# Kernel optimization log

Measured on AMD Instinct MI355X. Metric: run time of the kernel, lower is better.

## Reference

```python
import jax, jax.numpy as jnp
import numpy as np

N_NODES = 50000
N_EDGES = 800000
D_IN = 128
H = 4
D_HEAD = 32
NEG_SLOPE = 0.2


def _weighted_agg(h, w, src, dst, n):
    # agg[dst] += h[src] * w  (DGL update_all with weighted_message/reduce)
    return jax.ops.segment_sum(h[src] * w[:, None], dst, num_segments=n)


def _gat_conv(h, W, al, ar, b, src, dst):
    # DGL GATConv (eval mode: dropout off), activation=None, bias=True
    n = h.shape[0]
    feat = (h @ W).reshape(n, H, D_HEAD)          # [N,H,D]
    el = jnp.sum(feat * al, axis=-1)               # [N,H]
    er = jnp.sum(feat * ar, axis=-1)               # [N,H]
    e = jax.nn.leaky_relu(el[src] + er[dst], NEG_SLOPE)  # [E,H]
    # edge softmax over incoming edges of each dst node, per head
    m = jax.ops.segment_max(e, dst, num_segments=n)      # [N,H]
    ee = jnp.exp(e - m[dst])
    s = jax.ops.segment_sum(ee, dst, num_segments=n)     # [N,H]
    alpha = ee / s[dst]                                   # [E,H]
    msg = feat[src] * alpha[:, :, None]                   # [E,H,D]
    rst = jax.ops.segment_sum(msg, dst, num_segments=n)   # [N,H,D]
    rst = rst + b.reshape(1, H, D_HEAD)
    return rst.reshape(n, H * D_HEAD)                     # flatten(1)


def setup_inputs() -> dict:
    key = jax.random.key(0)
    ks = jax.random.split(key, 12)
    inp = {
        "in_feat": jax.random.normal(ks[0], (N_NODES, D_IN), dtype=jnp.float32),
        "edge_weights": jax.random.uniform(ks[1], (N_EDGES,), dtype=jnp.float32),
        "W0": jax.random.normal(ks[2], (D_IN, H * D_HEAD), dtype=jnp.float32) * (1.0 / np.sqrt(D_IN)),
        "al0": jax.random.normal(ks[3], (H, D_HEAD), dtype=jnp.float32) * 0.1,
        "ar0": jax.random.normal(ks[4], (H, D_HEAD), dtype=jnp.float32) * 0.1,
        "b0": jnp.zeros((H * D_HEAD,), dtype=jnp.float32),
        "W1": jax.random.normal(ks[5], (H * D_HEAD, H * D_HEAD), dtype=jnp.float32) * (1.0 / np.sqrt(H * D_HEAD)),
        "al1": jax.random.normal(ks[6], (H, D_HEAD), dtype=jnp.float32) * 0.1,
        "ar1": jax.random.normal(ks[7], (H, D_HEAD), dtype=jnp.float32) * 0.1,
        "b1": jnp.zeros((H * D_HEAD,), dtype=jnp.float32),
        "src": jax.random.randint(ks[8], (N_EDGES,), 0, N_NODES, dtype=jnp.int32),
        "dst": jax.random.randint(ks[9], (N_EDGES,), 0, N_NODES, dtype=jnp.int32),
    }
    return inp


def reference(in_feat, edge_weights, W0, al0, ar0, b0, W1, al1, ar1, b1, src, dst):
    n = in_feat.shape[0]
    h = in_feat
    # hidden layer (layers[:-1]) with edge-weighted aggregation + residual + relu
    h_old = h
    h = h + _weighted_agg(h, edge_weights, src, dst, n)
    h = _gat_conv(h, W0, al0, ar0, b0, src, dst)
    h = h + h_old  # residual=True
    h = jax.nn.relu(h)
    # final layer
    h = h + _weighted_agg(h, edge_weights, src, dst, n)
    h = _gat_conv(h, W1, al1, ar1, b1, src, dst)
    return h
```

## Files before the change

### kernel.cpp

```cpp
#include <hip/hip_runtime.h>

#define NN 50000
#define NE 800000
#define D 128
#define NH 4
#define NB 391

typedef __attribute__((ext_vector_type(8))) short bf16x8;
typedef __attribute__((ext_vector_type(4))) float f32x4;

__device__ __forceinline__ float lrelu(float x){ return x > 0.f ? x : 0.2f*x; }
__device__ __forceinline__ float sel4(int h, float4 v){
  float r = v.x;
  r = (h==1)? v.y : r;
  r = (h==2)? v.z : r;
  r = (h==3)? v.w : r;
  return r;
}
__device__ __forceinline__ ushort f2bf(float f){
  union{ float f; uint i;} v; v.f=f;
  uint r = v.i + 0x7FFFu + ((v.i>>16)&1u);
  return (ushort)(r>>16);
}
__device__ __forceinline__ uint pack2bf(float x, float y){
  return (uint)f2bf(x) | ((uint)f2bf(y)<<16);
}
__device__ __forceinline__ float bflo(uint u){ return __uint_as_float(u<<16); }
__device__ __forceinline__ float bfhi(uint u){ return __uint_as_float(u & 0xffff0000u); }
__device__ __forceinline__ uint encf(float f){
  uint b = __float_as_uint(f);
  return (b & 0x80000000u) ? ~b : (b | 0x80000000u);
}
__device__ __forceinline__ float decf(uint e){
  return (e & 0x80000000u) ? __uint_as_float(e ^ 0x80000000u) : __uint_as_float(~e);
}


__global__ void k_bhist(const int* __restrict__ dst, int* __restrict__ bcnt){
  __shared__ int c[NB];
  int t = threadIdx.x;
  for (int i=t;i<NB;i+=256) c[i]=0;
  __syncthreads();
  int base = blockIdx.x*4096;
  #pragma unroll
  for (int k=0;k<16;k++){
    int i = base + k*256 + t;
    if (i<NE) atomicAdd(&c[dst[i]>>7], 1);
  }
  __syncthreads();
  for (int i=t;i<NB;i+=256){ int v=c[i]; if (v) atomicAdd(&bcnt[i], v); }
}

__global__ void k_bscan(const int* __restrict__ bcnt, int* __restrict__ boff, int* __restrict__ bcur){
  __shared__ int sd[512];
  int t = threadIdx.x;
  int own = (t<NB)? bcnt[t] : 0;
  sd[t] = own;
  __syncthreads();
  for (int off=1; off<512; off<<=1){
    int v = (t>=off)? sd[t-off] : 0;
    __syncthreads();
    sd[t] += v;
    __syncthreads();
  }
  if (t<NB){
    int excl = sd[t]-own;
    boff[t]=excl; bcur[t]=excl;
  }
  if (t==0) boff[NB]=NE;
}

__global__ void k_binscat(const int* __restrict__ src, const int* __restrict__ dst,
                          const float* __restrict__ w, int* __restrict__ bcur,
                          uint2* __restrict__ stg){
  __shared__ int cnt[NB];
  __shared__ int st[NB];
  int t = threadIdx.x;
  for (int i=t;i<NB;i+=256) cnt[i]=0;
  __syncthreads();
  int base = blockIdx.x*4096;
  #pragma unroll
  for (int k=0;k<16;k++){
    int i = base + k*256 + t;
    if (i<NE) atomicAdd(&cnt[dst[i]>>7], 1);
  }
  __syncthreads();
  for (int i=t;i<NB;i+=256){
    int c = cnt[i];
    st[i] = c ? atomicAdd(&bcur[i], c) : 0;
    cnt[i] = 0;
  }
  __syncthreads();
  #pragma unroll
  for (int k=0;k<16;k++){
    int i = base + k*256 + t;
    if (i<NE){
      int d = dst[i];
      int b = d>>7;
      int pos = st[b] + atomicAdd(&cnt[b], 1);
      stg[pos] = make_uint2((uint)src[i] | ((uint)d<<16), __float_as_uint(w[i]));
    }
  }
}

__global__ void k_bfinal(const uint2* __restrict__ stg, const int* __restrict__ boff,
                         int* __restrict__ offs, uint2* __restrict__ edge_s){
  int b = blockIdx.x, t = threadIdx.x;
  int beg = boff[b], end = boff[b+1];
  int node0 = b<<7;
  int nnode = NN - node0; if (nnode>128) nnode=128;
  __shared__ int cnt[128];
  __shared__ int cur[128];
  if (t<128) cnt[t]=0;
  __syncthreads();
  for (int j=beg+t; j<end; j+=256)
    atomicAdd(&cnt[(stg[j].x>>16)&127], 1);
  __syncthreads();
  int own = (t<128)? cnt[t] : 0;
  for (int off=1; off<128; off<<=1){
    int v = (t<128 && t>=off)? cnt[t-off] : 0;
    __syncthreads();
    if (t<128) cnt[t] += v;
    __syncthreads();
  }
  if (t<128){
    int excl = cnt[t]-own;
    cur[t] = beg + excl;
    if (t<nnode) offs[node0+t] = beg + excl;
  }
  if (b==NB-1 && t==0) offs[NN]=NE;
  __syncthreads();
  for (int j=beg+t; j<end; j+=256){
    uint2 v = stg[j];
    int pos = atomicAdd(&cur[(v.x>>16)&127], 1);
    edge_s[pos] = v;
  }
}


__global__ void k_cvt(const float* __restrict__ in, uint* __restrict__ out16, int n2){
  int i = blockIdx.x*256 + threadIdx.x;
  if (i < n2){
    float2 f = *(const float2*)&in[(size_t)i*2];
    out16[i] = pack2bf(f.x, f.y);
  }
}

__global__ void k_cvtW(const float* __restrict__ W, uint* __restrict__ Wt){
  int i = blockIdx.x*256 + threadIdx.x;
  if (i < 128*64){
    int n = i>>6, k2 = i&63;
    float a = W[(size_t)(2*k2)*128 + n];
    float b = W[(size_t)(2*k2+1)*128 + n];
    Wt[i] = pack2bf(a,b);
  }
}

__global__ void k_prep(const float* __restrict__ W0, const float* __restrict__ al0,
                       const float* __restrict__ ar0, const float* __restrict__ W1,
                       const float* __restrict__ al1, const float* __restrict__ ar1,
                       uint* __restrict__ aug0, uint* __restrict__ aug1){
  __shared__ float sv[128][4];
  int b = blockIdx.x, t = threadIdx.x;
  const float* W = (b<2)? W0 : W1;
  const float* a = (b==0)? al0 : (b==1)? ar0 : (b==2)? al1 : ar1;
  uint* o = (b<2)? aug0 : aug1;
  int rbase = (b&1)? 132 : 128;
  int d = t>>2, h = t&3;
  float s = 0.f;
  #pragma unroll
  for (int i=0;i<32;i++) s += W[d*128 + h*32 + i] * a[h*32 + i];
  sv[d][h] = s;
  __syncthreads();
  if (t<256){
    int h2 = t>>6, k2 = t&63;
    o[(rbase+h2)*64 + k2] = pack2bf(sv[2*k2][h2], sv[2*k2+1][h2]);
  }
}

__global__ void k_wagg(const float* __restrict__ hinF, const uint* __restrict__ hin16,
                       const int* __restrict__ offs, const uint2* __restrict__ edge_s,
                       uint* __restrict__ xout16){
  int node = (blockIdx.x*256 + threadIdx.x)>>6;
  int lane = threadIdx.x & 63;
  if (node>=NN) return;
  int beg=offs[node], end=offs[node+1];
  int half = lane>>5, li = lane&31;
  float a0=0.f,a1=0.f,a2=0.f,a3=0.f;
  if (half==0){
    if (hinF){
      float4 s4 = *(const float4*)&hinF[(size_t)node*D + li*4];
      a0=s4.x; a1=s4.y; a2=s4.z; a3=s4.w;
    } else {
      uint2 su = *(const uint2*)&hin16[(size_t)node*64 + li*2];
      a0=bflo(su.x); a1=bfhi(su.x); a2=bflo(su.y); a3=bfhi(su.y);
    }
  }
  for (int cb=beg; cb<end; cb+=64){
    int n = end-cb; if (n>64) n=64;
    int idx = cb + (lane<n ? lane : n-1);
    uint2 ed = edge_s[idx];
    int sp = (int)(ed.x & 0xffffu);
    float wp = __uint_as_float(ed.y);
    int iters = (n+1)>>1;
    for (int i0=0; i0<iters; i0+=8){
      uint2 u[8]; float wk[8];
      #pragma unroll
      for (int k=0;k<8;k++){
        int q = 2*(i0+k) + half;
        int sj = __shfl(sp, q & 63);
        float wq = __shfl(wp, q & 63);
        wk[k] = (q<n)? wq : 0.f;
        u[k] = *(const uint2*)&hin16[(size_t)sj*64 + li*2];
      }
      #pragma unroll
      for (int k=0;k<8;k++){
        a0 = fmaf(bflo(u[k].x), wk[k], a0);
        a1 = fmaf(bfhi(u[k].x), wk[k], a1);
        a2 = fmaf(bflo(u[k].y), wk[k], a2);
        a3 = fmaf(bfhi(u[k].y), wk[k], a3);
      }
    }
  }
  a0 += __shfl_xor(a0,32); a1 += __shfl_xor(a1,32);
  a2 += __shfl_xor(a2,32); a3 += __shfl_xor(a3,32);
  if (half==0){
    uint2 o; o.x = pack2bf(a0,a1); o.y = pack2bf(a2,a3);
    *(uint2*)&xout16[(size_t)node*64 + li*2] = o;
  }
}

__global__ __launch_bounds__(256) void k_gemm(const uint* __restrict__ X16, const uint* __restrict__ Wtaug,
    uint* __restrict__ feat16, float* __restrict__ el, float* __restrict__ er,
    uint* __restrict__ gmax_u){
  __shared__ uint sX[128*64];
  __shared__ uint sW[144*64];
  __shared__ float sgm[4][4];
  int t = threadIdx.x;
  int row0 = blockIdx.x*128;
  #pragma unroll
  for (int i=0;i<8;i++){
    int idx = t + 256*i;
    int r = idx>>4, cb = idx&15;
    int gr = row0 + r;
    uint4 v = make_uint4(0u,0u,0u,0u);
    if (gr < NN) v = *(const uint4*)&X16[(size_t)gr*64 + cb*4];
    *(uint4*)&sX[r*64 + ((cb*4) ^ ((r&7)<<2))] = v;
  }
  #pragma unroll
  for (int i=0;i<9;i++){
    int idx = t + 256*i;
    int r = idx>>4, cb = idx&15;
    uint4 v = *(const uint4*)&Wtaug[(size_t)r*64 + cb*4];
    *(uint4*)&sW[r*64 + ((cb*4) ^ ((r&7)<<2))] = v;
  }
  __syncthreads();
  int w = t>>6, l = t&63;
  int lr = l&15, lk = l>>4;
  f32x4 acc[2][8];
  f32x4 acc_e[2];
  #pragma unroll
  for (int rf=0;rf<2;rf++){
    acc_e[rf] = (f32x4){0.f,0.f,0.f,0.f};
    #pragma unroll
    for (int cf=0;cf<8;cf++) acc[rf][cf] = (f32x4){0.f,0.f,0.f,0.f};
  }
  #pragma unroll
  for (int ks=0; ks<4; ks++){
    int cb = ks*4 + lk;
    bf16x8 a[2], b[8], baug;
    #pragma unroll
    for (int rf=0;rf<2;rf++){
      int r = w*32 + rf*16 + lr;
      a[rf] = *(const bf16x8*)&sX[r*64 + ((cb*4) ^ ((r&7)<<2))];
    }
    #pragma unroll
    for (int cf=0;cf<8;cf++){
      int r = cf*16 + lr;
      b[cf] = *(const bf16x8*)&sW[r*64 + ((cb*4) ^ ((r&7)<<2))];
    }
    {
      int r = 128 + lr;
      baug = *(const bf16x8*)&sW[r*64 + ((cb*4) ^ ((r&7)<<2))];
    }
    #pragma unroll
    for (int rf=0;rf<2;rf++){
      #pragma unroll
      for (int cf=0;cf<8;cf++)
        acc[rf][cf] = __builtin_amdgcn_mfma_f32_16x16x32_bf16(a[rf], b[cf], acc[rf][cf], 0,0,0);
      acc_e[rf] = __builtin_amdgcn_mfma_f32_16x16x32_bf16(a[rf], baug, acc_e[rf], 0,0,0);
    }
  }
  ushort* f16s = (ushort*)feat16;
  float gm = -3e38f;
  #pragma unroll
  for (int rf=0;rf<2;rf++){
    #pragma unroll
    for (int reg=0;reg<4;reg++){
      int grow = row0 + w*32 + rf*16 + lk*4 + reg;
      if (grow < NN){
        #pragma unroll
        for (int cf=0;cf<8;cf++)
          f16s[(size_t)grow*128 + cf*16 + lr] = f2bf(acc[rf][cf][reg]);
        float v = acc_e[rf][reg];
        if (lr<4){ el[grow*4 + lr] = v; gm = fmaxf(gm, v); }
        else if (lr<8){ er[grow*4 + lr-4] = v; }
      }
    }
  }
  gm = fmaxf(gm, __shfl_xor(gm,16));
  gm = fmaxf(gm, __shfl_xor(gm,32));
  if (l<4) sgm[w][l] = gm;
  __syncthreads();
  if (t<4){
    float m = fmaxf(fmaxf(sgm[0][t],sgm[1][t]), fmaxf(sgm[2][t],sgm[3][t]));
    atomicMax(&gmax_u[t], encf(m));
  }
}

template<int FINAL>
__global__ void k_gat(const uint* __restrict__ feat16, const float4* __restrict__ el4,
                      const float4* __restrict__ er4, const uint* __restrict__ gmax_u,
                      const float* __restrict__ bias, const int* __restrict__ offs,
                      const uint2* __restrict__ edge_s, const float* __restrict__ resid,
                      float* __restrict__ outF, uint* __restrict__ out16){
  int node = (blockIdx.x*256 + threadIdx.x)>>6;
  int lane = threadIdx.x & 63;
  if (node>=NN) return;
  int beg=offs[node], end=offs[node+1];
  int half = lane>>5, li = lane&31;
  int hF = li>>3;
  int hp = lane & 3;
  int eidx = lane>>2;
  float4 erv = er4[node];
  uint4 g = *(const uint4*)gmax_u;
  float4 m4 = make_float4(lrelu(decf(g.x)+erv.x), lrelu(decf(g.y)+erv.y),
                          lrelu(decf(g.z)+erv.z), lrelu(decf(g.w)+erv.w));
  float mh  = sel4(hp, m4);
  float erh = sel4(hp, erv);
  float s_acc = 0.f;
  float a0=0.f,a1=0.f,a2=0.f,a3=0.f;
  for (int cb=beg; cb<end; cb+=16){
    int n = end-cb; if (n>16) n=16;
    int jj = cb + (eidx<n ? eidx : n-1);
    uint2 ed = edge_s[jj];
    int sp = (int)(ed.x & 0xffffu);
    float4 ev = el4[sp];
    float e = __expf(lrelu(sel4(hp,ev)+erh) - mh);
    e = (eidx<n) ? e : 0.f;
    s_acc += e;
    uint2 u[8]; float eh[8];
    #pragma unroll
    for (int k=0;k<8;k++){
      int bidx = (2*k + half)<<2;
      int sj = __shfl(sp, bidx);
      eh[k] = __shfl(e, bidx + hF);
      u[k] = *(const uint2*)&feat16[(size_t)sj*64 + li*2];
    }
    #pragma unroll
    for (int k=0;k<8;k++){
      a0 = fmaf(bflo(u[k].x), eh[k], a0);
      a1 = fmaf(bfhi(u[k].x), eh[k], a1);
      a2 = fmaf(bflo(u[k].y), eh[k], a2);
      a3 = fmaf(bfhi(u[k].y), eh[k], a3);
    }
  }
  s_acc += __shfl_xor(s_acc,4);
  s_acc += __shfl_xor(s_acc,8);
  s_acc += __shfl_xor(s_acc,16);
  s_acc += __shfl_xor(s_acc,32);
  float sh = __shfl(s_acc, hF);
  a0 += __shfl_xor(a0,32); a1 += __shfl_xor(a1,32);
  a2 += __shfl_xor(a2,32); a3 += __shfl_xor(a3,32);
  if (half==0){
    float inv = (end>beg)? 1.f/sh : 0.f;
    float4 bv = *(const float4*)&bias[li*4];
    float r0 = a0*inv + bv.x;
    float r1 = a1*inv + bv.y;
    float r2 = a2*inv + bv.z;
    float r3 = a3*inv + bv.w;
    if (FINAL==0){
      float4 rs = *(const float4*)&resid[(size_t)node*D + li*4];
      r0 = fmaxf(r0+rs.x, 0.f);
      r1 = fmaxf(r1+rs.y, 0.f);
      r2 = fmaxf(r2+rs.z, 0.f);
      r3 = fmaxf(r3+rs.w, 0.f);
      uint2 o16; o16.x = pack2bf(r0,r1); o16.y = pack2bf(r2,r3);
      *(uint2*)&out16[(size_t)node*64 + li*2] = o16;
    } else {
      *(float4*)&outF[(size_t)node*D + li*4] = make_float4(r0,r1,r2,r3);
    }
  }
}

extern "C" void kernel_launch(void* const* d_in, const int* in_sizes, int n_in,
                              void* d_out, int out_size, void* d_ws, size_t ws_size,
                              hipStream_t stream){
  const float* in_feat = (const float*)d_in[0];
  const float* ew  = (const float*)d_in[1];
  const float* W0  = (const float*)d_in[2];
  const float* al0 = (const float*)d_in[3];
  const float* ar0 = (const float*)d_in[4];
  const float* b0  = (const float*)d_in[5];
  const float* W1  = (const float*)d_in[6];
  const float* al1 = (const float*)d_in[7];
  const float* ar1 = (const float*)d_in[8];
  const float* b1  = (const float*)d_in[9];
  const int* src = (const int*)d_in[10];
  const int* dst = (const int*)d_in[11];
  float* out = (float*)d_out;

  char* p = (char*)d_ws;
  auto alloc = [&](size_t b)->void*{ void* r=(void*)p; p += ((b+255)&~(size_t)255); return r; };
  int*   offs   = (int*)alloc((size_t)(NN+1)*4);
  int*   bcnt   = (int*)alloc((size_t)NB*4);
  int*   boff   = (int*)alloc((size_t)(NB+1)*4);
  int*   bcur   = (int*)alloc((size_t)NB*4);
  uint2* stg    = (uint2*)alloc((size_t)NE*8);
  uint2* edge_s = (uint2*)alloc((size_t)NE*8);
  uint*  h16    = (uint*)alloc((size_t)NN*64*4);
  uint*  x16    = (uint*)alloc((size_t)NN*64*4);
  uint*  feat16 = (uint*)alloc((size_t)NN*64*4);
  uint*  Wt0    = (uint*)alloc((size_t)144*64*4);
  uint*  Wt1    = (uint*)alloc((size_t)144*64*4);
  float* el     = (float*)alloc((size_t)NN*NH*4);
  float* er     = (float*)alloc((size_t)NN*NH*4);
  uint*  gmax0  = (uint*)alloc(16);
  uint*  gmax1  = (uint*)alloc(16);

  hipMemsetAsync(bcnt, 0, (size_t)NB*4, stream);
  hipMemsetAsync(gmax0, 0, 16, stream);
  hipMemsetAsync(gmax1, 0, 16, stream);
  hipMemsetAsync(Wt0, 0, (size_t)144*64*4, stream);
  hipMemsetAsync(Wt1, 0, (size_t)144*64*4, stream);
  int nsb = (NE + 4095)/4096;
  k_bhist<<<nsb,256,0,stream>>>(dst, bcnt);
  k_bscan<<<1,512,0,stream>>>(bcnt, boff, bcur);
  k_binscat<<<nsb,256,0,stream>>>(src, dst, ew, bcur, stg);
  k_bfinal<<<NB,256,0,stream>>>(stg, boff, offs, edge_s);
  k_cvt<<<(NN*64+255)/256,256,0,stream>>>(in_feat, h16, NN*64);
  k_cvtW<<<(128*64+255)/256,256,0,stream>>>(W0, Wt0);
  k_cvtW<<<(128*64+255)/256,256,0,stream>>>(W1, Wt1);
  k_prep<<<4,512,0,stream>>>(W0, al0, ar0, W1, al1, ar1, Wt0, Wt1);

  int nwb = (NN*64 + 255)/256;
  int ngb = (NN+127)/128;

  k_wagg<<<nwb,256,0,stream>>>(in_feat, h16, offs, edge_s, x16);
  k_gemm<<<ngb,256,0,stream>>>(x16, Wt0, feat16, el, er, gmax0);
  k_gat<0><<<nwb,256,0,stream>>>(feat16, (const float4*)el, (const float4*)er, gmax0, b0,
                                 offs, edge_s, in_feat, nullptr, h16);
  k_wagg<<<nwb,256,0,stream>>>(nullptr, h16, offs, edge_s, x16);
  k_gemm<<<ngb,256,0,stream>>>(x16, Wt1, feat16, el, er, gmax1);
  k_gat<1><<<nwb,256,0,stream>>>(feat16, (const float4*)el, (const float4*)er, gmax1, b1,
                                 offs, edge_s, nullptr, out, nullptr);
}
```

Before: 234.8 us.

## Slice feature aggregation by column chunks and split GAT softmax into separate pass

Aggregation kernels are rewritten so each block handles one 16-column slice (32 bytes) of four nodes, with blockIdx ordered so consecutive blocks cover different slices. The aim is to shrink the working set of gathered rows per pass and improve L2 locality. Edges are compacted to 4-byte src|fp16-weight words. GAT softmax weights are precomputed per head into an fp16 packed array by a new k_soft kernel. This adds an extra pass and extra global traffic, and fp16 weights lose some precision.

```diff
diff --git a/kernel.cpp b/kernel.cpp
--- a/kernel.cpp
+++ b/kernel.cpp
@@ -1,4 +1,5 @@
 #include <hip/hip_runtime.h>
+#include <hip/hip_fp16.h>
 
 #define NN 50000
 #define NE 800000
@@ -34,6 +35,8 @@
 __device__ __forceinline__ float decf(uint e){
   return (e & 0x80000000u) ? __uint_as_float(e ^ 0x80000000u) : __uint_as_float(~e);
 }
+__device__ __forceinline__ uint f2h(float f){ return (uint)__half_as_ushort(__float2half(f)); }
+__device__ __forceinline__ float h2f(uint u){ return __half2float(__ushort_as_half((ushort)u)); }
 
 
 __global__ void k_bhist(const int* __restrict__ dst, int* __restrict__ bcnt){
@@ -104,7 +107,7 @@
 }
 
 __global__ void k_bfinal(const uint2* __restrict__ stg, const int* __restrict__ boff,
-                         int* __restrict__ offs, uint2* __restrict__ edge_s){
+                         int* __restrict__ offs, uint* __restrict__ wpack){
   int b = blockIdx.x, t = threadIdx.x;
   int beg = boff[b], end = boff[b+1];
   int node0 = b<<7;
@@ -133,17 +136,18 @@
   for (int j=beg+t; j<end; j+=256){
     uint2 v = stg[j];
     int pos = atomicAdd(&cur[(v.x>>16)&127], 1);
-    edge_s[pos] = v;
-  }
-}
-
-
-__global__ void k_cvt(const float* __restrict__ in, uint* __restrict__ out16, int n2){
-  int i = blockIdx.x*256 + threadIdx.x;
-  if (i < n2){
-    float2 f = *(const float2*)&in[(size_t)i*2];
-    out16[i] = pack2bf(f.x, f.y);
-  }
+    wpack[pos] = (v.x & 0xffffu) | (f2h(__uint_as_float(v.y))<<16);
+  }
+}
+
+
+__global__ void k_cvt_slice(const float* __restrict__ in, uint* __restrict__ out16){
+  int slice = blockIdx.x & 7;
+  int id = (blockIdx.x>>3)*256 + threadIdx.x;
+  if (id >= NN*8) return;
+  int v = id>>3, cp = id&7;
+  float2 f = *(const float2*)&in[(size_t)v*D + slice*16 + cp*2];
+  out16[(size_t)v*64 + slice*8 + cp] = pack2bf(f.x, f.y);
 }
 
 __global__ void k_cvtW(const float* __restrict__ W, uint* __restrict__ Wt){
@@ -178,56 +182,40 @@
   }
 }
 
-__global__ void k_wagg(const float* __restrict__ hinF, const uint* __restrict__ hin16,
-                       const int* __restrict__ offs, const uint2* __restrict__ edge_s,
-                       uint* __restrict__ xout16){
-  int node = (blockIdx.x*256 + threadIdx.x)>>6;
+__global__ void k_wagg_slice(const float* __restrict__ hinF, const uint* __restrict__ hin16,
+                             const int* __restrict__ offs, const uint* __restrict__ wpack,
+                             uint* __restrict__ x16){
+  int slice = blockIdx.x & 7;
+  int node = ((blockIdx.x>>3)<<2) + (threadIdx.x>>6);
   int lane = threadIdx.x & 63;
   if (node>=NN) return;
+  int eg = lane>>3, cp = lane&7;
   int beg=offs[node], end=offs[node+1];
-  int half = lane>>5, li = lane&31;
-  float a0=0.f,a1=0.f,a2=0.f,a3=0.f;
-  if (half==0){
+  uint co = (uint)slice*32 + cp*4;
+  const char* hb = (const char*)hin16;
+  float a0=0.f, a1=0.f;
+  if (eg==0){
     if (hinF){
-      float4 s4 = *(const float4*)&hinF[(size_t)node*D + li*4];
-      a0=s4.x; a1=s4.y; a2=s4.z; a3=s4.w;
+      float2 s2 = *(const float2*)&hinF[(size_t)node*D + slice*16 + cp*2];
+      a0=s2.x; a1=s2.y;
     } else {
-      uint2 su = *(const uint2*)&hin16[(size_t)node*64 + li*2];
-      a0=bflo(su.x); a1=bfhi(su.x); a2=bflo(su.y); a3=bfhi(su.y);
-    }
-  }
-  for (int cb=beg; cb<end; cb+=64){
-    int n = end-cb; if (n>64) n=64;
-    int idx = cb + (lane<n ? lane : n-1);
-    uint2 ed = edge_s[idx];
-    int sp = (int)(ed.x & 0xffffu);
-    float wp = __uint_as_float(ed.y);
-    int iters = (n+1)>>1;
-    for (int i0=0; i0<iters; i0+=8){
-      uint2 u[8]; float wk[8];
-      #pragma unroll
-      for (int k=0;k<8;k++){
-        int q = 2*(i0+k) + half;
-        int sj = __shfl(sp, q & 63);
-        float wq = __shfl(wp, q & 63);
-        wk[k] = (q<n)? wq : 0.f;
-        u[k] = *(const uint2*)&hin16[(size_t)sj*64 + li*2];
-      }
-      #pragma unroll
-      for (int k=0;k<8;k++){
-        a0 = fmaf(bflo(u[k].x), wk[k], a0);
-        a1 = fmaf(bfhi(u[k].x), wk[k], a1);
-        a2 = fmaf(bflo(u[k].y), wk[k], a2);
-        a3 = fmaf(bfhi(u[k].y), wk[k], a3);
-      }
-    }
-  }
+      uint su = hin16[(size_t)node*64 + slice*8 + cp];
+      a0=bflo(su); a1=bfhi(su);
+    }
+  }
+  for (int cb=beg; cb<end; cb+=8){
+    int j = cb + eg;
+    uint wp = wpack[j<end ? j : end-1];
+    float w = (j<end)? h2f(wp>>16) : 0.f;
+    uint u = *(const uint*)(hb + ((wp & 0xffffu)*256u + co));
+    a0 = fmaf(bflo(u), w, a0);
+    a1 = fmaf(bfhi(u), w, a1);
+  }
+  a0 += __shfl_xor(a0,8);  a1 += __shfl_xor(a1,8);
+  a0 += __shfl_xor(a0,16); a1 += __shfl_xor(a1,16);
   a0 += __shfl_xor(a0,32); a1 += __shfl_xor(a1,32);
-  a2 += __shfl_xor(a2,32); a3 += __shfl_xor(a3,32);
-  if (half==0){
-    uint2 o; o.x = pack2bf(a0,a1); o.y = pack2bf(a2,a3);
-    *(uint2*)&xout16[(size_t)node*64 + li*2] = o;
-  }
+  if (eg==0)
+    x16[(size_t)node*64 + slice*8 + cp] = pack2bf(a0,a1);
 }
 
 __global__ __launch_bounds__(256) void k_gemm(const uint* __restrict__ X16, const uint* __restrict__ Wtaug,
@@ -318,20 +306,15 @@
   }
 }
 
-template<int FINAL>
-__global__ void k_gat(const uint* __restrict__ feat16, const float4* __restrict__ el4,
-                      const float4* __restrict__ er4, const uint* __restrict__ gmax_u,
-                      const float* __restrict__ bias, const int* __restrict__ offs,
-                      const uint2* __restrict__ edge_s, const float* __restrict__ resid,
-                      float* __restrict__ outF, uint* __restrict__ out16){
+__global__ void k_soft(const int* __restrict__ offs, const uint* __restrict__ wpack,
+                       const float4* __restrict__ el4, const float4* __restrict__ er4,
+                       const uint* __restrict__ gmax_u,
+                       uint* __restrict__ epack, float* __restrict__ s4){
   int node = (blockIdx.x*256 + threadIdx.x)>>6;
   int lane = threadIdx.x & 63;
   if (node>=NN) return;
+  int eidx = lane>>2, hp = lane&3;
   int beg=offs[node], end=offs[node+1];
-  int half = lane>>5, li = lane&31;
-  int hF = li>>3;
-  int hp = lane & 3;
-  int eidx = lane>>2;
   float4 erv = er4[node];
   uint4 g = *(const uint4*)gmax_u;
   float4 m4 = make_float4(lrelu(decf(g.x)+erv.x), lrelu(decf(g.y)+erv.y),
@@ -339,56 +322,62 @@
   float mh  = sel4(hp, m4);
   float erh = sel4(hp, erv);
   float s_acc = 0.f;
-  float a0=0.f,a1=0.f,a2=0.f,a3=0.f;
   for (int cb=beg; cb<end; cb+=16){
     int n = end-cb; if (n>16) n=16;
-    int jj = cb + (eidx<n ? eidx : n-1);
-    uint2 ed = edge_s[jj];
-    int sp = (int)(ed.x & 0xffffu);
-    float4 ev = el4[sp];
-    float e = __expf(lrelu(sel4(hp,ev)+erh) - mh);
-    e = (eidx<n) ? e : 0.f;
-    s_acc += e;
-    uint2 u[8]; float eh[8];
-    #pragma unroll
-    for (int k=0;k<8;k++){
-      int bidx = (2*k + half)<<2;
-      int sj = __shfl(sp, bidx);
-      eh[k] = __shfl(e, bidx + hF);
-      u[k] = *(const uint2*)&feat16[(size_t)sj*64 + li*2];
-    }
-    #pragma unroll
-    for (int k=0;k<8;k++){
-      a0 = fmaf(bflo(u[k].x), eh[k], a0);
-      a1 = fmaf(bfhi(u[k].x), eh[k], a1);
-      a2 = fmaf(bflo(u[k].y), eh[k], a2);
-      a3 = fmaf(bfhi(u[k].y), eh[k], a3);
+    int j = cb + (eidx<n ? eidx : n-1);
+    uint src = wpack[j] & 0xffffu;
+    float e = __expf(lrelu(sel4(hp, el4[src])+erh) - mh);
+    if (eidx<n){
+      s_acc += e;
+      epack[hp*NE + j] = src | (f2h(e)<<16);
     }
   }
   s_acc += __shfl_xor(s_acc,4);
   s_acc += __shfl_xor(s_acc,8);
   s_acc += __shfl_xor(s_acc,16);
   s_acc += __shfl_xor(s_acc,32);
-  float sh = __shfl(s_acc, hF);
+  if (lane<4) s4[node*4 + lane] = s_acc;
+}
+
+template<int FINAL>
+__global__ void k_gat_slice(const uint* __restrict__ feat16, const uint* __restrict__ epack,
+                            const float* __restrict__ s4, const float* __restrict__ bias,
+                            const int* __restrict__ offs, const float* __restrict__ resid,
+                            float* __restrict__ outF, uint* __restrict__ out16){
+  int slice = blockIdx.x & 7;
+  int node = ((blockIdx.x>>3)<<2) + (threadIdx.x>>6);
+  int lane = threadIdx.x & 63;
+  if (node>=NN) return;
+  int eg = lane>>3, cp = lane&7;
+  int head = slice>>1;
+  const uint* ep = epack + (size_t)head*NE;
+  int beg=offs[node], end=offs[node+1];
+  uint co = (uint)slice*32 + cp*4;
+  const char* fbb = (const char*)feat16;
+  float a0=0.f, a1=0.f;
+  for (int cb=beg; cb<end; cb+=8){
+    int j = cb + eg;
+    uint pk = ep[j<end ? j : end-1];
+    float e = (j<end)? h2f(pk>>16) : 0.f;
+    uint u = *(const uint*)(fbb + ((pk & 0xffffu)*256u + co));
+    a0 = fmaf(bflo(u), e, a0);
+    a1 = fmaf(bfhi(u), e, a1);
+  }
+  a0 += __shfl_xor(a0,8);  a1 += __shfl_xor(a1,8);
+  a0 += __shfl_xor(a0,16); a1 += __shfl_xor(a1,16);
   a0 += __shfl_xor(a0,32); a1 += __shfl_xor(a1,32);
-  a2 += __shfl_xor(a2,32); a3 += __shfl_xor(a3,32);
-  if (half==0){
-    float inv = (end>beg)? 1.f/sh : 0.f;
-    float4 bv = *(const float4*)&bias[li*4];
-    float r0 = a0*inv + bv.x;
-    float r1 = a1*inv + bv.y;
-    float r2 = a2*inv + bv.z;
-    float r3 = a3*inv + bv.w;
+  if (eg==0){
+    float inv = (end>beg)? 1.f/s4[node*4 + head] : 0.f;
+    int col = slice*16 + cp*2;
+    float r0 = a0*inv + bias[col];
+    float r1 = a1*inv + bias[col+1];
     if (FINAL==0){
-      float4 rs = *(const float4*)&resid[(size_t)node*D + li*4];
+      float2 rs = *(const float2*)&resid[(size_t)node*D + col];
       r0 = fmaxf(r0+rs.x, 0.f);
       r1 = fmaxf(r1+rs.y, 0.f);
-      r2 = fmaxf(r2+rs.z, 0.f);
-      r3 = fmaxf(r3+rs.w, 0.f);
-      uint2 o16; o16.x = pack2bf(r0,r1); o16.y = pack2bf(r2,r3);
-      *(uint2*)&out16[(size_t)node*64 + li*2] = o16;
+      out16[(size_t)node*64 + slice*8 + cp] = pack2bf(r0,r1);
     } else {
-      *(float4*)&outF[(size_t)node*D + li*4] = make_float4(r0,r1,r2,r3);
+      *(float2*)&outF[(size_t)node*D + col] = make_float2(r0,r1);
     }
   }
 }
@@ -417,7 +406,9 @@
   int*   boff   = (int*)alloc((size_t)(NB+1)*4);
   int*   bcur   = (int*)alloc((size_t)NB*4);
   uint2* stg    = (uint2*)alloc((size_t)NE*8);
-  uint2* edge_s = (uint2*)alloc((size_t)NE*8);
+  uint*  wpack  = (uint*)alloc((size_t)NE*4);
+  uint*  epack  = (uint*)alloc((size_t)NE*4*NH);
+  float* s4     = (float*)alloc((size_t)NN*NH*4);
   uint*  h16    = (uint*)alloc((size_t)NN*64*4);
   uint*  x16    = (uint*)alloc((size_t)NN*64*4);
   uint*  feat16 = (uint*)alloc((size_t)NN*64*4);
@@ -437,21 +428,23 @@
   k_bhist<<<nsb,256,0,stream>>>(dst, bcnt);
   k_bscan<<<1,512,0,stream>>>(bcnt, boff, bcur);
   k_binscat<<<nsb,256,0,stream>>>(src, dst, ew, bcur, stg);
-  k_bfinal<<<NB,256,0,stream>>>(stg, boff, offs, edge_s);
-  k_cvt<<<(NN*64+255)/256,256,0,stream>>>(in_feat, h16, NN*64);
+  k_bfinal<<<NB,256,0,stream>>>(stg, boff, offs, wpack);
+  int ncv = 8*((NN*8 + 255)/256);
+  k_cvt_slice<<<ncv,256,0,stream>>>(in_feat, h16);
   k_cvtW<<<(128*64+255)/256,256,0,stream>>>(W0, Wt0);
   k_cvtW<<<(128*64+255)/256,256,0,stream>>>(W1, Wt1);
   k_prep<<<4,512,0,stream>>>(W0, al0, ar0, W1, al1, ar1, Wt0, Wt1);
 
-  int nwb = (NN*64 + 255)/256;
-  int ngb = (NN+127)/128;
-
-  k_wagg<<<nwb,256,0,stream>>>(in_feat, h16, offs, edge_s, x16);
+  int nslc = 8*((NN+3)/4);
+  int nwb  = (NN*64 + 255)/256;
+  int ngb  = (NN+127)/128;
+
+  k_wagg_slice<<<nslc,256,0,stream>>>(in_feat, h16, offs, wpack, x16);
   k_gemm<<<ngb,256,0,stream>>>(x16, Wt0, feat16, el, er, gmax0);
-  k_gat<0><<<nwb,256,0,stream>>>(feat16, (const float4*)el, (const float4*)er, gmax0, b0,
-                                 offs, edge_s, in_feat, nullptr, h16);
-  k_wagg<<<nwb,256,0,stream>>>(nullptr, h16, offs, edge_s, x16);
+  k_soft<<<nwb,256,0,stream>>>(offs, wpack, (const float4*)el, (const float4*)er, gmax0, epack, s4);
+  k_gat_slice<0><<<nslc,256,0,stream>>>(feat16, epack, s4, b0, offs, in_feat, nullptr, h16);
+  k_wagg_slice<<<nslc,256,0,stream>>>(nullptr, h16, offs, wpack, x16);
   k_gemm<<<ngb,256,0,stream>>>(x16, Wt1, feat16, el, er, gmax1);
-  k_gat<1><<<nwb,256,0,stream>>>(feat16, (const float4*)el, (const float4*)er, gmax1, b1,
-                                 offs, edge_s, nullptr, out, nullptr);
-}
+  k_soft<<<nwb,256,0,stream>>>(offs, wpack, (const float4*)el, (const float4*)er, gmax1, epack, s4);
+  k_gat_slice<1><<<nslc,256,0,stream>>>(feat16, epack, s4, b1, offs, nullptr, out, nullptr);
+}
```

Result: slower. 733.1 us (+212.3%).

## Pack edge src and fp16 weight into one word; prefetch next edge chunk in GAT

Applied to the files above, without the earlier changes.

Sorted edges are stored as a single 32-bit word holding the 16-bit source index and an fp16 edge weight, replacing the 8-byte record. This halves edge-stream traffic in the aggregation and attention kernels. Gather addresses become 32-bit byte offsets instead of 64-bit index arithmetic. The GAT kernel also software-pipelines the loop, loading the next chunk's edge word and el values before the FMAs of the current chunk. The cost is fp16 rounding of the edge weights.

```diff
diff --git a/kernel.cpp b/kernel.cpp
--- a/kernel.cpp
+++ b/kernel.cpp
@@ -1,4 +1,5 @@
 #include <hip/hip_runtime.h>
+#include <hip/hip_fp16.h>
 
 #define NN 50000
 #define NE 800000
@@ -34,6 +35,8 @@
 __device__ __forceinline__ float decf(uint e){
   return (e & 0x80000000u) ? __uint_as_float(e ^ 0x80000000u) : __uint_as_float(~e);
 }
+__device__ __forceinline__ uint f2h(float f){ return (uint)__half_as_ushort(__float2half(f)); }
+__device__ __forceinline__ float h2f(uint u){ return __half2float(__ushort_as_half((ushort)u)); }
 
 
 __global__ void k_bhist(const int* __restrict__ dst, int* __restrict__ bcnt){
@@ -104,7 +107,7 @@
 }
 
 __global__ void k_bfinal(const uint2* __restrict__ stg, const int* __restrict__ boff,
-                         int* __restrict__ offs, uint2* __restrict__ edge_s){
+                         int* __restrict__ offs, uint* __restrict__ wpack){
   int b = blockIdx.x, t = threadIdx.x;
   int beg = boff[b], end = boff[b+1];
   int node0 = b<<7;
@@ -133,7 +136,7 @@
   for (int j=beg+t; j<end; j+=256){
     uint2 v = stg[j];
     int pos = atomicAdd(&cur[(v.x>>16)&127], 1);
-    edge_s[pos] = v;
+    wpack[pos] = (v.x & 0xffffu) | (f2h(__uint_as_float(v.y))<<16);
   }
 }
 
@@ -179,13 +182,15 @@
 }
 
 __global__ void k_wagg(const float* __restrict__ hinF, const uint* __restrict__ hin16,
-                       const int* __restrict__ offs, const uint2* __restrict__ edge_s,
+                       const int* __restrict__ offs, const uint* __restrict__ wpack,
                        uint* __restrict__ xout16){
   int node = (blockIdx.x*256 + threadIdx.x)>>6;
   int lane = threadIdx.x & 63;
   if (node>=NN) return;
   int beg=offs[node], end=offs[node+1];
   int half = lane>>5, li = lane&31;
+  const char* hb = (const char*)hin16;
+  uint li8 = li*8;
   float a0=0.f,a1=0.f,a2=0.f,a3=0.f;
   if (half==0){
     if (hinF){
@@ -199,19 +204,19 @@
   for (int cb=beg; cb<end; cb+=64){
     int n = end-cb; if (n>64) n=64;
     int idx = cb + (lane<n ? lane : n-1);
-    uint2 ed = edge_s[idx];
-    int sp = (int)(ed.x & 0xffffu);
-    float wp = __uint_as_float(ed.y);
+    uint ed = wpack[idx];
+    uint spo = (ed & 0xffffu)<<8;
+    float wp = h2f(ed>>16);
     int iters = (n+1)>>1;
     for (int i0=0; i0<iters; i0+=8){
       uint2 u[8]; float wk[8];
       #pragma unroll
       for (int k=0;k<8;k++){
         int q = 2*(i0+k) + half;
-        int sj = __shfl(sp, q & 63);
+        uint so = __shfl(spo, q & 63);
         float wq = __shfl(wp, q & 63);
         wk[k] = (q<n)? wq : 0.f;
-        u[k] = *(const uint2*)&hin16[(size_t)sj*64 + li*2];
+        u[k] = *(const uint2*)(hb + (so + li8));
       }
       #pragma unroll
       for (int k=0;k<8;k++){
@@ -322,7 +327,7 @@
 __global__ void k_gat(const uint* __restrict__ feat16, const float4* __restrict__ el4,
                       const float4* __restrict__ er4, const uint* __restrict__ gmax_u,
                       const float* __restrict__ bias, const int* __restrict__ offs,
-                      const uint2* __restrict__ edge_s, const float* __restrict__ resid,
+                      const uint* __restrict__ wpack, const float* __restrict__ resid,
                       float* __restrict__ outF, uint* __restrict__ out16){
   int node = (blockIdx.x*256 + threadIdx.x)>>6;
   int lane = threadIdx.x & 63;
@@ -332,6 +337,8 @@
   int hF = li>>3;
   int hp = lane & 3;
   int eidx = lane>>2;
+  const char* fb = (const char*)feat16;
+  uint li8 = li*8;
   float4 erv = er4[node];
   uint4 g = *(const uint4*)gmax_u;
   float4 m4 = make_float4(lrelu(decf(g.x)+erv.x), lrelu(decf(g.y)+erv.y),
@@ -340,29 +347,41 @@
   float erh = sel4(hp, erv);
   float s_acc = 0.f;
   float a0=0.f,a1=0.f,a2=0.f,a3=0.f;
-  for (int cb=beg; cb<end; cb+=16){
-    int n = end-cb; if (n>16) n=16;
-    int jj = cb + (eidx<n ? eidx : n-1);
-    uint2 ed = edge_s[jj];
-    int sp = (int)(ed.x & 0xffffu);
-    float4 ev = el4[sp];
-    float e = __expf(lrelu(sel4(hp,ev)+erh) - mh);
-    e = (eidx<n) ? e : 0.f;
-    s_acc += e;
-    uint2 u[8]; float eh[8];
-    #pragma unroll
-    for (int k=0;k<8;k++){
-      int bidx = (2*k + half)<<2;
-      int sj = __shfl(sp, bidx);
-      eh[k] = __shfl(e, bidx + hF);
-      u[k] = *(const uint2*)&feat16[(size_t)sj*64 + li*2];
-    }
-    #pragma unroll
-    for (int k=0;k<8;k++){
-      a0 = fmaf(bflo(u[k].x), eh[k], a0);
-      a1 = fmaf(bfhi(u[k].x), eh[k], a1);
-      a2 = fmaf(bflo(u[k].y), eh[k], a2);
-      a3 = fmaf(bfhi(u[k].y), eh[k], a3);
+  if (beg < end){
+    int cb = beg;
+    int n = end-beg; if (n>16) n=16;
+    uint ed = wpack[beg + (eidx<n ? eidx : n-1)];
+    float4 ev = el4[ed & 0xffffu];
+    while (1){
+      uint spo = (ed & 0xffffu)<<8;
+      float e = __expf(lrelu(sel4(hp,ev)+erh) - mh);
+      e = (eidx<n) ? e : 0.f;
+      s_acc += e;
+      uint2 u[8]; float eh[8];
+      #pragma unroll
+      for (int k=0;k<8;k++){
+        int bidx = (2*k + half)<<2;
+        uint so = __shfl(spo, bidx);
+        eh[k] = __shfl(e, bidx + hF);
+        u[k] = *(const uint2*)(fb + (so + li8));
+      }
+      int cb2 = cb + 16;
+      int n2 = 0; uint ed2 = 0u;
+      float4 ev2 = make_float4(0.f,0.f,0.f,0.f);
+      if (cb2 < end){
+        n2 = end-cb2; if (n2>16) n2=16;
+        ed2 = wpack[cb2 + (eidx<n2 ? eidx : n2-1)];
+        ev2 = el4[ed2 & 0xffffu];
+      }
+      #pragma unroll
+      for (int k=0;k<8;k++){
+        a0 = fmaf(bflo(u[k].x), eh[k], a0);
+        a1 = fmaf(bfhi(u[k].x), eh[k], a1);
+        a2 = fmaf(bflo(u[k].y), eh[k], a2);
+        a3 = fmaf(bfhi(u[k].y), eh[k], a3);
+      }
+      if (cb2 >= end) break;
+      cb = cb2; n = n2; ed = ed2; ev = ev2;
     }
   }
   s_acc += __shfl_xor(s_acc,4);
@@ -417,7 +436,7 @@
   int*   boff   = (int*)alloc((size_t)(NB+1)*4);
   int*   bcur   = (int*)alloc((size_t)NB*4);
   uint2* stg    = (uint2*)alloc((size_t)NE*8);
-  uint2* edge_s = (uint2*)alloc((size_t)NE*8);
+  uint*  wpack  = (uint*)alloc((size_t)NE*4);
   uint*  h16    = (uint*)alloc((size_t)NN*64*4);
   uint*  x16    = (uint*)alloc((size_t)NN*64*4);
   uint*  feat16 = (uint*)alloc((size_t)NN*64*4);
@@ -437,7 +456,7 @@
   k_bhist<<<nsb,256,0,stream>>>(dst, bcnt);
   k_bscan<<<1,512,0,stream>>>(bcnt, boff, bcur);
   k_binscat<<<nsb,256,0,stream>>>(src, dst, ew, bcur, stg);
-  k_bfinal<<<NB,256,0,stream>>>(stg, boff, offs, edge_s);
+  k_bfinal<<<NB,256,0,stream>>>(stg, boff, offs, wpack);
   k_cvt<<<(NN*64+255)/256,256,0,stream>>>(in_feat, h16, NN*64);
   k_cvtW<<<(128*64+255)/256,256,0,stream>>>(W0, Wt0);
   k_cvtW<<<(128*64+255)/256,256,0,stream>>>(W1, Wt1);
@@ -446,12 +465,12 @@
   int nwb = (NN*64 + 255)/256;
   int ngb = (NN+127)/128;
 
-  k_wagg<<<nwb,256,0,stream>>>(in_feat, h16, offs, edge_s, x16);
+  k_wagg<<<nwb,256,0,stream>>>(in_feat, h16, offs, wpack, x16);
   k_gemm<<<ngb,256,0,stream>>>(x16, Wt0, feat16, el, er, gmax0);
   k_gat<0><<<nwb,256,0,stream>>>(feat16, (const float4*)el, (const float4*)er, gmax0, b0,
-                                 offs, edge_s, in_feat, nullptr, h16);
-  k_wagg<<<nwb,256,0,stream>>>(nullptr, h16, offs, edge_s, x16);
+                                 offs, wpack, in_feat, nullptr, h16);
+  k_wagg<<<nwb,256,0,stream>>>(nullptr, h16, offs, wpack, x16);
   k_gemm<<<ngb,256,0,stream>>>(x16, Wt1, feat16, el, er, gmax1);
   k_gat<1><<<nwb,256,0,stream>>>(feat16, (const float4*)el, (const float4*)er, gmax1, b1,
-                                 offs, edge_s, nullptr, out, nullptr);
-}
+                                 offs, wpack, nullptr, out, nullptr);
+}
```

Measured after the change: 235.5 us. No clear change (+0.3%).
